# Kernel tuning notes

Hardware: AMD Instinct MI355X
Metric: run time of the kernel (lower is better)

The kernel has to match this reference:

```python
import jax, jax.numpy as jnp
import numpy as np

# Model dims (from CerebroOriginal defaults)
B, C, T, E, H, NB, NC = 256, 14, 8, 180, 5, 6, 4
DH = E // H          # 36
S = C * T            # 112 tokens
MLP = 4 * E          # 720


def qdq(x):
    """Int8 per-tensor fake quant-dequant (Brevitas Int8ActPerTensorFloat-style), STE."""
    s = jnp.maximum(jnp.max(jnp.abs(x)) / 127.0, 1e-8)
    y = jnp.clip(jnp.round(x / s), -128.0, 127.0) * s
    return x + jax.lax.stop_gradient(y - x)


def ln(x, g, b):
    m = jnp.mean(x, axis=-1, keepdims=True)
    v = jnp.var(x, axis=-1, keepdims=True)
    return (x - m) * jax.lax.rsqrt(v + 1e-5) * g + b


def qlinear(x, w, b):
    """QuantLinear: int8 input quant + int8 per-tensor weight quant, float bias."""
    return qdq(x) @ qdq(w).T + b


def setup_inputs() -> dict:
    key = jax.random.key(0)
    ks = jax.random.split(key, 16)
    r = lambda k, sh: (0.05 * jax.random.normal(k, sh)).astype(jnp.float32)
    f32 = jnp.float32
    return {
        "x": jax.random.normal(ks[0], (B, C, T), dtype=f32),
        "proj_w": r(ks[1], (E, C)), "proj_b": jnp.zeros((E,), f32),
        "ln1_g": jnp.ones((NB, E), f32), "ln1_b": jnp.zeros((NB, E), f32),
        "wq": r(ks[2], (NB, E, E)), "bq": jnp.zeros((NB, E), f32),
        "wk": r(ks[3], (NB, E, E)), "bk": jnp.zeros((NB, E), f32),
        "wv": r(ks[4], (NB, E, E)), "bv": jnp.zeros((NB, E), f32),
        "wo": r(ks[5], (NB, E, E)), "bo": jnp.zeros((NB, E), f32),
        "ln2_g": jnp.ones((NB, E), f32), "ln2_b": jnp.zeros((NB, E), f32),
        "fc1_w": r(ks[6], (NB, MLP, E)), "fc1_b": jnp.zeros((NB, MLP), f32),
        "fc2_w": r(ks[7], (NB, E, MLP)), "fc2_b": jnp.zeros((NB, E), f32),
        "fn_g": jnp.ones((E,), f32), "fn_b": jnp.zeros((E,), f32),
        "cls_w": r(ks[8], (NC, E)), "cls_b": jnp.zeros((NC,), f32),
    }


def forward(x, proj_w, proj_b, ln1_g, ln1_b, wq, bq, wk, bk, wv, bv, wo, bo,
            ln2_g, ln2_b, fc1_w, fc1_b, fc2_w, fc2_b, fn_g, fn_b, cls_w, cls_b):
    # input quant -> [B,T,C] -> proj -> [B,T,E]
    h = jnp.transpose(qdq(x), (0, 2, 1))
    h = qlinear(h, proj_w, proj_b)
    # expand over channels then flatten to [B, C*T, E] (channel-major token layout)
    h = jnp.broadcast_to(h[:, None], (B, C, T, E)).reshape(B, S, E)

    for i in range(NB):
        # --- attention sub-block ---
        r1 = h
        a = qdq(ln(h, ln1_g[i], ln1_b[i])).reshape(B, C, T, E)
        if i % 2 == 0:  # temporal attention: attend over T within each channel
            a = a.reshape(B * C, T, E)
            L = T
        else:           # channel attention: attend over C within each time step
            a = jnp.transpose(a, (0, 2, 1, 3)).reshape(B * T, C, E)
            L = C
        q = qlinear(a, wq[i], bq[i]).reshape(-1, L, H, DH)
        k = qlinear(a, wk[i], bk[i]).reshape(-1, L, H, DH)
        v = qlinear(a, wv[i], bv[i]).reshape(-1, L, H, DH)
        scores = jnp.einsum('nlhd,nmhd->nhlm', q, k) / jnp.sqrt(jnp.float32(DH))
        att = jax.nn.softmax(scores, axis=-1)
        o = jnp.einsum('nhlm,nmhd->nlhd', att, v).reshape(-1, L, E)
        o = qlinear(o, wo[i], bo[i])
        if i % 2 == 0:
            o = o.reshape(B, C, T, E)
        else:
            o = jnp.transpose(o.reshape(B, T, C, E), (0, 2, 1, 3))
        h = r1 + o.reshape(B, S, E)

        # --- MLP sub-block ---
        r2 = h
        m = qdq(ln(h, ln2_g[i], ln2_b[i]))
        m = qlinear(m, fc1_w[i], fc1_b[i])
        m = qdq(jax.nn.gelu(m))
        m = qlinear(m, fc2_w[i], fc2_b[i])
        h = r2 + m

    h = qdq(ln(h, fn_g, fn_b))
    pooled = jnp.mean(h, axis=1)                 # QuantMean over tokens -> [B, E]
    return qlinear(pooled, cls_w, cls_b)         # [B, NC]


def reference(x, proj_w, proj_b, ln1_g, ln1_b, wq, bq, wk, bk, wv, bv, wo, bo,
              ln2_g, ln2_b, fc1_w, fc1_b, fc2_w, fc2_b, fn_g, fn_b, cls_w, cls_b):
    return forward(x, proj_w, proj_b, ln1_g, ln1_b, wq, bq, wk, bk, wv, bv, wo, bo,
                   ln2_g, ln2_b, fc1_w, fc1_b, fc2_w, fc2_b, fn_g, fn_b, cls_w, cls_b)
```

## Files before the change

### kernel.cpp

```cpp
#include <hip/hip_runtime.h>
#include <math.h>

#define E 180
#define S 112
#define Bb 256
#define CC 14
#define TT 8
#define HH 5
#define DH 36
#define NBLK 6
#define MLPD 720
#define M_TOK (Bb*S)
#define BUF ((size_t)M_TOK * E)

#define KP1 192
#define KP2 736

#define WQ8_OFF   0
#define WK8_OFF   36864
#define WV8_OFF   73728
#define WO8_OFF   110592
#define FC18_OFF  147456
#define FC28_OFF  285696
#define WBLK      427008

#define SLOT_X    0
#define SLOT_PW   1
#define SLOT_CW   2
#define SLOT_POOL 3
#define SLOT_FLN  4
#define SLOT_WQ   8
#define SLOT_WK   16
#define SLOT_WV   24
#define SLOT_WO   32
#define SLOT_FC1  40
#define SLOT_FC2  48
#define SLOT_LN1  56
#define SLOT_O    64
#define SLOT_LN2  72
#define SLOT_GELU 80
#define SLOT_GXMAX 88
#define SLOT_GXA   96
#define SLOT_GXB   104
#define SLOT_GDIR  112

#define XL (-0.7535)
#define XR (-0.7515)

typedef unsigned long long ull;
typedef __attribute__((ext_vector_type(8))) short short8;
typedef __attribute__((ext_vector_type(4))) float f32x4;

__device__ __forceinline__ double slot_scale(const ull* s){
  return fmax(__longlong_as_double((long long)*s) / 127.0, 1e-8);
}
__device__ __forceinline__ void atomic_max_d(ull* p, double v){
  atomicMax(p, (ull)__double_as_longlong(v));
}
__device__ __forceinline__ ull enc_d(double d){
  ull b = (ull)__double_as_longlong(d);
  return (b >> 63) ? ~b : (b | 0x8000000000000000ULL);
}
__device__ __forceinline__ double dec_d(ull k){
  ull b = (k >> 63) ? (k ^ 0x8000000000000000ULL) : ~k;
  return __longlong_as_double((long long)b);
}
__device__ __forceinline__ float q_int_d(double x, double s){
  double r = rint(x / s);
  r = fmin(fmax(r, -128.0), 127.0);
  return (float)r;
}
__device__ __forceinline__ float q_int_fast(double x, double s, float sf){
  float t = (float)x / sf;
  float r = rintf(t);
  if(fabsf(t - r) > 0.497f || fabsf(t) > 126.f){
    double rd = rint(x / s);
    rd = fmin(fmax(rd, -128.0), 127.0);
    return (float)rd;
  }
  return r;
}
__device__ __forceinline__ unsigned short f2bf(float f){
  return (unsigned short)(__float_as_uint(f) >> 16);
}
__device__ __forceinline__ double gelu_d(double x){
  double t = tanh(0.7978845608028654*(x + 0.044715*x*x*x));
  return 0.5*x*(1.0 + t);
}
__device__ __forceinline__ float gelu_f(float x){
  float t = tanhf(0.7978845608f*(x + 0.044715f*x*x*x));
  return 0.5f*x*(1.f + t);
}
__device__ __forceinline__ int pmap(int row, int mode){
  if(mode == 0) return row;
  int b = row / S; int r = row - b*S; int t = r / CC; int c = r - t*CC;
  return b*S + c*TT + t;
}
__device__ __forceinline__ int pmap_inv(int row){
  int b = row / S; int r = row - b*S; int c = r / TT; int t = r - c*TT;
  return b*S + t*CC + c;
}

__global__ void init_slots(ull* slots){
  int t = threadIdx.x;
  slots[t] = (t >= SLOT_GXB && t < SLOT_GXB + NBLK) ? ~0ULL : 0ULL;
}

__global__ void amax_f32(const float* __restrict__ src, int seglen, ull* slots){
  int seg = blockIdx.y;
  const float* p = src + (size_t)seg * seglen;
  float m = 0.f;
  for(int i = blockIdx.x*256 + threadIdx.x; i < seglen; i += gridDim.x*256)
    m = fmaxf(m, fabsf(p[i]));
  __shared__ float red[256];
  red[threadIdx.x] = m;
  __syncthreads();
  for(int off = 128; off > 0; off >>= 1){
    if(threadIdx.x < off) red[threadIdx.x] = fmaxf(red[threadIdx.x], red[threadIdx.x+off]);
    __syncthreads();
  }
  if(threadIdx.x == 0) atomic_max_d(slots + seg, (double)red[0]);
}

__global__ void quant_w(const float* __restrict__ src, int N, int K,
                        int Npad, int Kpad, const ull* __restrict__ slotbase,
                        unsigned short* __restrict__ dst, size_t dstoff){
  int i = blockIdx.y;
  int e = blockIdx.x*256 + threadIdx.x;
  int tot = Npad * Kpad;
  if(e >= tot) return;
  int n = e / Kpad, k = e - n*Kpad;
  double s = slot_scale(slotbase + i);
  float val = 0.f;
  if(n < N && k < K)
    val = q_int_d((double)src[(size_t)i*N*K + (size_t)n*K + k], s);
  dst[(size_t)i*WBLK + dstoff + e] = f2bf(val);
}

__global__ void proj_bcast(const float* __restrict__ x, const float* __restrict__ pw,
                           const float* __restrict__ pb, double* __restrict__ h,
                           const ull* __restrict__ sx_slot,
                           const ull* __restrict__ sw_slot){
  int tid = blockIdx.x*256 + threadIdx.x;
  if(tid >= Bb*TT*E) return;
  int e = tid % E; int bt = tid / E; int t = bt % TT; int b = bt / TT;
  double sx = slot_scale(sx_slot), sw = slot_scale(sw_slot);
  float acc = 0.f;
  for(int c = 0; c < CC; c++)
    acc += q_int_d((double)x[(b*CC + c)*TT + t], sx) * q_int_d((double)pw[e*CC + c], sw);
  double o = (double)acc * (sx * sw) + (double)pb[e];
  for(int c = 0; c < CC; c++)
    h[((size_t)b*S + c*TT + t)*E + e] = o;
}

__device__ __forceinline__ void ln_row(const double* __restrict__ in, size_t base, int lane,
    const float* __restrict__ g, const float* __restrict__ bta,
    double& y0, double& y1, double& y2){
  double x0 = in[base + lane];
  double x1 = in[base + lane + 64];
  double x2 = (lane < E - 128) ? in[base + lane + 128] : 0.0;
  double sum = x0 + x1 + x2;
  for(int m = 32; m > 0; m >>= 1) sum += __shfl_xor(sum, m);
  double mean = sum * (1.0 / E);
  double d0 = x0 - mean, d1 = x1 - mean;
  double d2 = (lane < E - 128) ? (x2 - mean) : 0.0;
  double vs = d0*d0 + d1*d1 + d2*d2;
  for(int m = 32; m > 0; m >>= 1) vs += __shfl_xor(vs, m);
  double inv = 1.0 / sqrt(vs * (1.0 / E) + 1e-5);
  y0 = d0*inv*(double)g[lane]      + (double)bta[lane];
  y1 = d1*inv*(double)g[lane+64]   + (double)bta[lane+64];
  y2 = (lane < E - 128) ? (d2*inv*(double)g[lane+128] + (double)bta[lane+128]) : 0.0;
}

template<bool WRITE>
__global__ void __launch_bounds__(256) ln_amax(const double* __restrict__ in,
    double* __restrict__ out, const float* __restrict__ g,
    const float* __restrict__ bta, ull* amax_slot){
  int wave = threadIdx.x >> 6, lane = threadIdx.x & 63;
  double amx = 0.0;
  for(int tok = blockIdx.x*4 + wave; tok < M_TOK; tok += gridDim.x*4){
    size_t base = (size_t)tok * E;
    double y0, y1, y2;
    ln_row(in, base, lane, g, bta, y0, y1, y2);
    if(WRITE){
      out[base + lane]      = y0;
      out[base + lane + 64] = y1;
      if(lane < E - 128) out[base + lane + 128] = y2;
    }
    amx = fmax(amx, fmax(fabs(y0), fabs(y1)));
    if(lane < E - 128) amx = fmax(amx, fabs(y2));
  }
  for(int m = 32; m > 0; m >>= 1) amx = fmax(amx, __shfl_xor(amx, m));
  __shared__ double red[4];
  if(lane == 0) red[wave] = amx;
  __syncthreads();
  if(threadIdx.x == 0){
    double m = fmax(fmax(red[0], red[1]), fmax(red[2], red[3]));
    atomic_max_d(amax_slot, m);
  }
}

template<int PERM>
__global__ void __launch_bounds__(256) ln_quant(const double* __restrict__ in,
    unsigned short* __restrict__ dst, const float* __restrict__ g,
    const float* __restrict__ bta, const ull* __restrict__ slot){
  int wave = threadIdx.x >> 6, lane = threadIdx.x & 63;
  double s = slot_scale(slot); float sf = (float)s;
  for(int tok = blockIdx.x*4 + wave; tok < M_TOK; tok += gridDim.x*4){
    size_t base = (size_t)tok * E;
    double y0, y1, y2;
    ln_row(in, base, lane, g, bta, y0, y1, y2);
    int d = PERM ? pmap_inv(tok) : tok;
    unsigned short* dr = dst + (size_t)d*KP1;
    dr[lane]       = f2bf(q_int_fast(y0, s, sf));
    dr[lane + 64]  = f2bf(q_int_fast(y1, s, sf));
    dr[lane + 128] = (lane < E - 128) ? f2bf(q_int_fast(y2, s, sf)) : (unsigned short)0;
  }
}

__global__ void __launch_bounds__(256) quant_act(const double* __restrict__ src,
                          unsigned short* __restrict__ dst,
                          const ull* __restrict__ slot){
  int tid = blockIdx.x*256 + threadIdx.x;
  if(tid >= M_TOK*KP1/8) return;
  int idx8 = tid*8;
  int row = idx8 / KP1, k0 = idx8 - row*KP1;
  double s = slot_scale(slot); float sf = (float)s;
  const double* sp = src + (size_t)row*E;
  unsigned short v[8];
  #pragma unroll
  for(int j = 0; j < 8; j++){
    int k = k0 + j;
    v[j] = (k < E) ? f2bf(q_int_fast(sp[k], s, sf)) : (unsigned short)0;
  }
  *reinterpret_cast<short8*>(dst + (size_t)row*KP1 + k0) = *reinterpret_cast<short8*>(v);
}

__global__ void __launch_bounds__(256) quant_mid(const float* __restrict__ midacc,
                          unsigned short* __restrict__ dst,
                          const ull* __restrict__ slotA, const ull* __restrict__ slotW,
                          const ull* __restrict__ slotG, const float* __restrict__ bias){
  int tid = blockIdx.x*256 + threadIdx.x;
  if(tid >= M_TOK*KP2/8) return;
  int idx8 = tid*8;
  int row = idx8 / KP2, k0 = idx8 - row*KP2;
  double sAW = slot_scale(slotA) * slot_scale(slotW);
  double sg = slot_scale(slotG);
  float sAWf = (float)sAW, sgf = (float)sg;
  const float* sp = midacc + (size_t)row*MLPD;
  unsigned short v[8];
  #pragma unroll
  for(int j = 0; j < 8; j++){
    int k = k0 + j;
    if(k < MLPD){
      float a = sp[k];
      float y = fmaf(a, sAWf, bias[k]);
      float gf = gelu_f(y);
      float t = gf / sgf;
      float r = rintf(t);
      if(fabsf(t - r) > 0.497f || fabsf(t) > 126.f){
        double outv = (double)a*sAW + (double)bias[k];
        double rd = rint(gelu_d(outv)/sg);
        rd = fmin(fmax(rd, -128.0), 127.0);
        r = (float)rd;
      }
      v[j] = f2bf(r);
    } else v[j] = 0;
  }
  *reinterpret_cast<short8*>(dst + (size_t)row*KP2 + k0) = *reinterpret_cast<short8*>(v);
}

__global__ void gelu_finalize(ull* slots, int i){
  if(threadIdx.x != 0) return;
  double am = 0.0;
  ull kx = slots[SLOT_GXMAX + i];
  if(kx){ double x = dec_d(kx); if(fabs(x) < 1e299) am = fabs(gelu_d(x)); }
  ull ka = slots[SLOT_GXA + i];
  if(ka){ double x = dec_d(ka); if(fabs(x) < 1e299) am = fmax(am, fabs(gelu_d(x))); }
  ull kb = slots[SLOT_GXB + i];
  if(kb != ~0ULL){ double x = dec_d(kb); if(fabs(x) < 1e299) am = fmax(am, fabs(gelu_d(x))); }
  am = fmax(am, __longlong_as_double((long long)slots[SLOT_GDIR + i]));
  slots[SLOT_GELU + i] = (ull)__double_as_longlong(am);
}

__global__ void __launch_bounds__(256) gemm_qkv(
    const unsigned short* __restrict__ A8,
    const unsigned short* __restrict__ Wq, float* __restrict__ outq)
{
  int sel = blockIdx.x;
  const unsigned short* W8 = Wq + (size_t)sel*36864;
  float* outF = outq + (size_t)sel*((size_t)M_TOK*E);
  int wave = threadIdx.x >> 6, lane = threadIdx.x & 63;
  int m0 = blockIdx.y*64 + wave*16;
  int lr = lane & 15, lg = lane >> 4;
  const unsigned short* Arow = A8 + (size_t)(m0 + lr)*KP1 + lg*8;
  const unsigned short* Wbase = W8 + (size_t)lr*KP1 + lg*8;
  f32x4 acc[12];
  #pragma unroll
  for(int j = 0; j < 12; j++) acc[j] = (f32x4){0.f,0.f,0.f,0.f};
  for(int kk = 0; kk < KP1/32; kk++){
    short8 a = *reinterpret_cast<const short8*>(Arow + kk*32);
    const unsigned short* Wp = Wbase + kk*32;
    #pragma unroll
    for(int j = 0; j < 12; j++){
      short8 b = *reinterpret_cast<const short8*>(Wp + (size_t)j*16*KP1);
      acc[j] = __builtin_amdgcn_mfma_f32_16x16x32_bf16(a, b, acc[j], 0, 0, 0);
    }
  }
  #pragma unroll
  for(int j = 0; j < 12; j++){
    int col = j*16 + lr;
    if(col >= E) continue;
    #pragma unroll
    for(int r = 0; r < 4; r++){
      int row = m0 + lg*4 + r;
      outF[(size_t)row*E + col] = acc[j][r];
    }
  }
}

template<int NT, int EPI>
__global__ void __launch_bounds__(256) gemm_mfma(
    const unsigned short* __restrict__ A8, int Kpad,
    const unsigned short* __restrict__ W8,
    const float* __restrict__ bias, int Nreal,
    float* __restrict__ outF, double* __restrict__ outH,
    const ull* __restrict__ slotA, const ull* __restrict__ slotW,
    ull* cand, int permOut)
{
  int wave = threadIdx.x >> 6, lane = threadIdx.x & 63;
  int m0 = blockIdx.y*64 + wave*16;
  int tbase = blockIdx.x*NT;
  int lr = lane & 15, lg = lane >> 4;
  const unsigned short* Arow = A8 + (size_t)(m0 + lr)*Kpad + lg*8;
  const unsigned short* Wbase = W8 + (size_t)(tbase*16 + lr)*Kpad + lg*8;
  f32x4 acc[NT];
  #pragma unroll
  for(int j = 0; j < NT; j++) acc[j] = (f32x4){0.f,0.f,0.f,0.f};
  int ksteps = Kpad >> 5;
  for(int kk = 0; kk < ksteps; kk++){
    short8 a = *reinterpret_cast<const short8*>(Arow + kk*32);
    const unsigned short* Wp = Wbase + kk*32;
    #pragma unroll
    for(int j = 0; j < NT; j++){
      short8 b = *reinterpret_cast<const short8*>(Wp + (size_t)j*16*Kpad);
      acc[j] = __builtin_amdgcn_mfma_f32_16x16x32_bf16(a, b, acc[j], 0, 0, 0);
    }
  }
  double sAW = slot_scale(slotA) * slot_scale(slotW);
  double xmax = -1e300, xa = -1e300, xb = 1e300, dir = 0.0;
  #pragma unroll
  for(int j = 0; j < NT; j++){
    int col = (tbase + j)*16 + lr;
    if(col >= Nreal) continue;
    #pragma unroll
    for(int r = 0; r < 4; r++){
      int row = m0 + lg*4 + r;
      float a = acc[j][r];
      if(EPI == 0){
        outF[(size_t)row*Nreal + col] = a;
      } else if(EPI == 1){
        double outv = (double)a * sAW + (double)bias[col];
        int orow = pmap(row, permOut);
        size_t idx = (size_t)orow*E + col;
        outH[idx] += outv;
      } else {
        double outv = (double)a * sAW + (double)bias[col];
        outF[(size_t)row*Nreal + col] = a;
        xmax = fmax(xmax, outv);
        if(outv <= XL) xa = fmax(xa, outv);
        else if(outv < XR) dir = fmax(dir, fabs(gelu_d(outv)));
        if(outv >= XR) xb = fmin(xb, outv);
      }
    }
  }
  if(EPI == 2){
    for(int m = 32; m > 0; m >>= 1){
      xmax = fmax(xmax, __shfl_xor(xmax, m));
      xa   = fmax(xa,   __shfl_xor(xa,   m));
      xb   = fmin(xb,   __shfl_xor(xb,   m));
      dir  = fmax(dir,  __shfl_xor(dir,  m));
    }
    __shared__ double r0[4], r1[4], r2[4], r3[4];
    if(lane == 0){ r0[wave]=xmax; r1[wave]=xa; r2[wave]=xb; r3[wave]=dir; }
    __syncthreads();
    if(threadIdx.x == 0){
      double M0=r0[0], A0=r1[0], B0=r2[0], D0=r3[0];
      for(int w = 1; w < 4; w++){
        M0 = fmax(M0, r0[w]); A0 = fmax(A0, r1[w]);
        B0 = fmin(B0, r2[w]); D0 = fmax(D0, r3[w]);
      }
      atomicMax(cand + SLOT_GXMAX, enc_d(M0));
      atomicMax(cand + SLOT_GXA,   enc_d(A0));
      atomicMin(cand + SLOT_GXB,   enc_d(B0));
      atomicMax(cand + SLOT_GDIR,  (ull)__double_as_longlong(D0));
    }
  }
}

__global__ void __launch_bounds__(64) attn_kernel(const float* __restrict__ qa,
    const float* __restrict__ ka, const float* __restrict__ va,
    double* __restrict__ o, int L,
    const float* __restrict__ bq, const float* __restrict__ bk,
    const float* __restrict__ bv,
    const ull* __restrict__ sLN, const ull* __restrict__ sWq,
    const ull* __restrict__ sWk, const ull* __restrict__ sWv,
    ull* amax_slot){
  __shared__ double qs[14*36], ks[14*36], vs[14*36];
  __shared__ double att[14*14];
  int tid = threadIdx.x;
  double sA = slot_scale(sLN);
  double dq = sA * slot_scale(sWq);
  double dk = sA * slot_scale(sWk);
  double dv = sA * slot_scale(sWv);
  double am = 0.0;
  for(int gseg = 0; gseg < 8; gseg++){
    int segid = blockIdx.x*8 + gseg;
    int n = segid / HH, hh = segid % HH;
    size_t rowbase = (size_t)n*L*E + hh*DH;
    for(int idx = tid; idx < L*DH; idx += 64){
      int l = idx / DH, d = idx - l*DH;
      size_t g = rowbase + (size_t)l*E + d;
      int bcol = hh*DH + d;
      qs[idx] = (double)qa[g]*dq + (double)bq[bcol];
      ks[idx] = (double)ka[g]*dk + (double)bk[bcol];
      vs[idx] = (double)va[g]*dv + (double)bv[bcol];
    }
    __syncthreads();
    for(int idx = tid; idx < L*L; idx += 64){
      int l = idx / L, m = idx - l*L;
      double s = 0.0;
      for(int d = 0; d < DH; d++) s += qs[l*DH+d] * ks[m*DH+d];
      att[idx] = s * (1.0 / 6.0);
    }
    __syncthreads();
    if(tid < L){
      double mx = -1e300;
      for(int m = 0; m < L; m++) mx = fmax(mx, att[tid*L+m]);
      double sm = 0.0;
      for(int m = 0; m < L; m++){ double e_ = exp(att[tid*L+m] - mx); att[tid*L+m] = e_; sm += e_; }
      double r = 1.0 / sm;
      for(int m = 0; m < L; m++) att[tid*L+m] *= r;
    }
    __syncthreads();
    for(int idx = tid; idx < L*DH; idx += 64){
      int l = idx / DH, d = idx - l*DH;
      double s = 0.0;
      for(int m = 0; m < L; m++) s += att[l*L+m] * vs[m*DH+d];
      o[rowbase + (size_t)l*E + d] = s;
      am = fmax(am, fabs(s));
    }
    __syncthreads();
  }
  for(int m = 32; m > 0; m >>= 1) am = fmax(am, __shfl_xor(am, m));
  if(tid == 0) atomic_max_d(amax_slot, am);
}

__global__ void __launch_bounds__(256) pooled_kernel(const double* __restrict__ lnout,
    double* __restrict__ pooled, const ull* __restrict__ slot_ln,
    ull* slot_pooled){
  int tid = blockIdx.x*256 + threadIdx.x;
  double am = 0.0;
  if(tid < Bb*E){
    int b = tid / E, e = tid - (tid/E)*E;
    double sl = slot_scale(slot_ln); float slf = (float)sl;
    double sum = 0.0;
    for(int s = 0; s < S; s++)
      sum += (double)q_int_fast(lnout[((size_t)b*S + s)*E + e], sl, slf) * sl;
    double pv = sum * (1.0 / S);
    pooled[(size_t)b*E + e] = pv;
    am = fabs(pv);
  }
  for(int m = 32; m > 0; m >>= 1) am = fmax(am, __shfl_xor(am, m));
  if((threadIdx.x & 63) == 0) atomic_max_d(slot_pooled, am);
}

__global__ void __launch_bounds__(64) cls_kernel(const double* __restrict__ pooled,
    const float* __restrict__ cw, const float* __restrict__ cb,
    float* __restrict__ out, const ull* __restrict__ sp,
    const ull* __restrict__ sw){
  int tid = blockIdx.x*64 + threadIdx.x;
  if(tid >= Bb*4) return;
  int b = tid >> 2, j = tid & 3;
  double s1 = slot_scale(sp), s2 = slot_scale(sw);
  float acc = 0.f;
  for(int e = 0; e < E; e++)
    acc += q_int_d(pooled[b*E + e], s1) * q_int_d((double)cw[j*E + e], s2);
  out[tid] = (float)((double)acc * (s1 * s2) + (double)cb[j]);
}

extern "C" void kernel_launch(void* const* d_in, const int* in_sizes, int n_in,
                              void* d_out, int out_size, void* d_ws, size_t ws_size,
                              hipStream_t stream){
  const float* x      = (const float*)d_in[0];
  const float* proj_w = (const float*)d_in[1];
  const float* proj_b = (const float*)d_in[2];
  const float* ln1_g  = (const float*)d_in[3];
  const float* ln1_b  = (const float*)d_in[4];
  const float* wq     = (const float*)d_in[5];
  const float* bq     = (const float*)d_in[6];
  const float* wk     = (const float*)d_in[7];
  const float* bk     = (const float*)d_in[8];
  const float* wv     = (const float*)d_in[9];
  const float* bv     = (const float*)d_in[10];
  const float* wo     = (const float*)d_in[11];
  const float* bo     = (const float*)d_in[12];
  const float* ln2_g  = (const float*)d_in[13];
  const float* ln2_b  = (const float*)d_in[14];
  const float* fc1_w  = (const float*)d_in[15];
  const float* fc1_b  = (const float*)d_in[16];
  const float* fc2_w  = (const float*)d_in[17];
  const float* fc2_b  = (const float*)d_in[18];
  const float* fn_g   = (const float*)d_in[19];
  const float* fn_b   = (const float*)d_in[20];
  const float* cls_w  = (const float*)d_in[21];
  const float* cls_b  = (const float*)d_in[22];
  float* outp = (float*)d_out;

  char* base = (char*)d_ws;
  ull*    slots  = (ull*)base;
  double* h      = (double*)(base + 4096);
  double* scr    = h + BUF;
  float*  facc   = (float*)(scr + BUF);
  float*  qacc   = facc;
  float*  midacc = facc;
  double* pooled = (double*)facc;
  unsigned short* act8 = (unsigned short*)(facc + (size_t)M_TOK*MLPD);
  unsigned short* mid8 = act8 + (size_t)M_TOK*KP1;
  unsigned short* w8   = mid8 + (size_t)M_TOK*KP2;

  init_slots<<<1, 128, 0, stream>>>(slots);

  amax_f32<<<dim3(32,1), 256, 0, stream>>>(x,      Bb*CC*TT, slots + SLOT_X);
  amax_f32<<<dim3(1,1),  256, 0, stream>>>(proj_w, E*CC,     slots + SLOT_PW);
  amax_f32<<<dim3(1,1),  256, 0, stream>>>(cls_w,  4*E,      slots + SLOT_CW);
  amax_f32<<<dim3(4,NBLK),  256, 0, stream>>>(wq,    E*E,    slots + SLOT_WQ);
  amax_f32<<<dim3(4,NBLK),  256, 0, stream>>>(wk,    E*E,    slots + SLOT_WK);
  amax_f32<<<dim3(4,NBLK),  256, 0, stream>>>(wv,    E*E,    slots + SLOT_WV);
  amax_f32<<<dim3(4,NBLK),  256, 0, stream>>>(wo,    E*E,    slots + SLOT_WO);
  amax_f32<<<dim3(16,NBLK), 256, 0, stream>>>(fc1_w, MLPD*E, slots + SLOT_FC1);
  amax_f32<<<dim3(16,NBLK), 256, 0, stream>>>(fc2_w, MLPD*E, slots + SLOT_FC2);

  quant_w<<<dim3((KP1*KP1+255)/256, NBLK), 256, 0, stream>>>(wq, E, E, KP1, KP1, slots+SLOT_WQ, w8, WQ8_OFF);
  quant_w<<<dim3((KP1*KP1+255)/256, NBLK), 256, 0, stream>>>(wk, E, E, KP1, KP1, slots+SLOT_WK, w8, WK8_OFF);
  quant_w<<<dim3((KP1*KP1+255)/256, NBLK), 256, 0, stream>>>(wv, E, E, KP1, KP1, slots+SLOT_WV, w8, WV8_OFF);
  quant_w<<<dim3((KP1*KP1+255)/256, NBLK), 256, 0, stream>>>(wo, E, E, KP1, KP1, slots+SLOT_WO, w8, WO8_OFF);
  quant_w<<<dim3((MLPD*KP1+255)/256, NBLK), 256, 0, stream>>>(fc1_w, MLPD, E, MLPD, KP1, slots+SLOT_FC1, w8, FC18_OFF);
  quant_w<<<dim3((KP1*KP2+255)/256, NBLK), 256, 0, stream>>>(fc2_w, E, MLPD, KP1, KP2, slots+SLOT_FC2, w8, FC28_OFF);

  proj_bcast<<<(Bb*TT*E + 255)/256, 256, 0, stream>>>(x, proj_w, proj_b, h,
                                                      slots + SLOT_X, slots + SLOT_PW);

  const int QA_GRID = (M_TOK*KP1/8 + 255)/256;
  const int QM_GRID = (M_TOK*KP2/8 + 255)/256;
  const int LN_GRID = 1792;

  for(int i = 0; i < NBLK; i++){
    int pi = i & 1;
    const unsigned short* wb = w8 + (size_t)i*WBLK;
    ln_amax<false><<<LN_GRID, 256, 0, stream>>>(h, nullptr, ln1_g + i*E, ln1_b + i*E, slots + SLOT_LN1 + i);
    if(pi == 0)
      ln_quant<0><<<LN_GRID, 256, 0, stream>>>(h, act8, ln1_g + i*E, ln1_b + i*E, slots + SLOT_LN1 + i);
    else
      ln_quant<1><<<LN_GRID, 256, 0, stream>>>(h, act8, ln1_g + i*E, ln1_b + i*E, slots + SLOT_LN1 + i);
    gemm_qkv<<<dim3(3, M_TOK/64), 256, 0, stream>>>(act8, wb + WQ8_OFF, qacc);
    int L = pi ? CC : TT;
    int nseg = (M_TOK/L)*HH;
    attn_kernel<<<nseg/8, 64, 0, stream>>>(qacc, qacc + (size_t)M_TOK*E, qacc + (size_t)2*M_TOK*E, scr, L,
        bq + i*E, bk + i*E, bv + i*E,
        slots+SLOT_LN1+i, slots+SLOT_WQ+i, slots+SLOT_WK+i, slots+SLOT_WV+i,
        slots + SLOT_O + i);
    quant_act<<<QA_GRID, 256, 0, stream>>>(scr, act8, slots + SLOT_O + i);
    gemm_mfma<12,1><<<dim3(1, M_TOK/64), 256, 0, stream>>>(act8, KP1, wb + WO8_OFF, bo + i*E, E,
        nullptr, h, slots+SLOT_O+i, slots+SLOT_WO+i, nullptr, pi);
    ln_amax<false><<<LN_GRID, 256, 0, stream>>>(h, nullptr, ln2_g + i*E, ln2_b + i*E, slots + SLOT_LN2 + i);
    ln_quant<0><<<LN_GRID, 256, 0, stream>>>(h, act8, ln2_g + i*E, ln2_b + i*E, slots + SLOT_LN2 + i);
    gemm_mfma<9,2><<<dim3(5, M_TOK/64), 256, 0, stream>>>(act8, KP1, wb + FC18_OFF, fc1_b + i*MLPD, MLPD,
        midacc, nullptr, slots+SLOT_LN2+i, slots+SLOT_FC1+i, slots + i, 0);
    gelu_finalize<<<1, 64, 0, stream>>>(slots, i);
    quant_mid<<<QM_GRID, 256, 0, stream>>>(midacc, mid8,
        slots+SLOT_LN2+i, slots+SLOT_FC1+i, slots+SLOT_GELU+i, fc1_b + i*MLPD);
    gemm_mfma<12,1><<<dim3(1, M_TOK/64), 256, 0, stream>>>(mid8, KP2, wb + FC28_OFF, fc2_b + i*E, E,
        nullptr, h, slots+SLOT_GELU+i, slots+SLOT_FC2+i, nullptr, 0);
  }

  ln_amax<true><<<LN_GRID, 256, 0, stream>>>(h, scr, fn_g, fn_b, slots + SLOT_FLN);
  pooled_kernel<<<(Bb*E + 255)/256, 256, 0, stream>>>(scr, pooled, slots + SLOT_FLN, slots + SLOT_POOL);
  cls_kernel<<<(Bb*4 + 63)/64, 64, 0, stream>>>(pooled, cls_w, cls_b, outp,
                                                slots + SLOT_POOL, slots + SLOT_CW);
}
```

Before: 3.880 ms.

## Fuse LayerNorm amax into residual GEMM epilogue and rewrite attention kernel

The residual-add GEMM epilogue (Wo and fc2) now computes the updated row, its LayerNorm, and the max-abs for the next LayerNorm's quant scale, then publishes it atomically. This removes the separate ln_amax passes over h inside the loop. Attention is templated on sequence length, stores Q/K/V in float shared memory, folds the dequant scale and bias algebraically into the score computation, pads the score rows, and handles 4 segments per block instead of 8. The risks are extra register pressure in the GEMM epilogue, because each row is kept in doubles for the reductions, and small numerical differences from the rearranged bias algebra.

Result: faster. 3.634 ms (-6.3%).

```diff
diff --git a/kernel.cpp b/kernel.cpp
--- a/kernel.cpp
+++ b/kernel.cpp
@@ -326,7 +326,8 @@
     const float* __restrict__ bias, int Nreal,
     float* __restrict__ outF, double* __restrict__ outH,
     const ull* __restrict__ slotA, const ull* __restrict__ slotW,
-    ull* cand, int permOut)
+    ull* cand, int permOut,
+    const float* __restrict__ lng, const float* __restrict__ lnb)
 {
   int wave = threadIdx.x >> 6, lane = threadIdx.x & 63;
   int m0 = blockIdx.y*64 + wave*16;
@@ -348,23 +349,25 @@
     }
   }
   double sAW = slot_scale(slotA) * slot_scale(slotW);
-  double xmax = -1e300, xa = -1e300, xb = 1e300, dir = 0.0;
-  #pragma unroll
-  for(int j = 0; j < NT; j++){
-    int col = (tbase + j)*16 + lr;
-    if(col >= Nreal) continue;
+  if(EPI == 0){
     #pragma unroll
-    for(int r = 0; r < 4; r++){
-      int row = m0 + lg*4 + r;
-      float a = acc[j][r];
-      if(EPI == 0){
-        outF[(size_t)row*Nreal + col] = a;
-      } else if(EPI == 1){
-        double outv = (double)a * sAW + (double)bias[col];
-        int orow = pmap(row, permOut);
-        size_t idx = (size_t)orow*E + col;
-        outH[idx] += outv;
-      } else {
+    for(int j = 0; j < NT; j++){
+      int col = (tbase + j)*16 + lr;
+      if(col >= Nreal) continue;
+      #pragma unroll
+      for(int r = 0; r < 4; r++)
+        outF[(size_t)(m0 + lg*4 + r)*Nreal + col] = acc[j][r];
+    }
+  } else if(EPI == 2){
+    double xmax = -1e300, xa = -1e300, xb = 1e300, dir = 0.0;
+    #pragma unroll
+    for(int j = 0; j < NT; j++){
+      int col = (tbase + j)*16 + lr;
+      if(col >= Nreal) continue;
+      #pragma unroll
+      for(int r = 0; r < 4; r++){
+        int row = m0 + lg*4 + r;
+        float a = acc[j][r];
         double outv = (double)a * sAW + (double)bias[col];
         outF[(size_t)row*Nreal + col] = a;
         xmax = fmax(xmax, outv);
@@ -373,8 +376,6 @@
         if(outv >= XR) xb = fmin(xb, outv);
       }
     }
-  }
-  if(EPI == 2){
     for(int m = 32; m > 0; m >>= 1){
       xmax = fmax(xmax, __shfl_xor(xmax, m));
       xa   = fmax(xa,   __shfl_xor(xa,   m));
@@ -395,58 +396,128 @@
       atomicMin(cand + SLOT_GXB,   enc_d(B0));
       atomicMax(cand + SLOT_GDIR,  (ull)__double_as_longlong(D0));
     }
-  }
-}
-
-__global__ void __launch_bounds__(64) attn_kernel(const float* __restrict__ qa,
+  } else {
+    double amx = 0.0;
+    #pragma unroll
+    for(int r = 0; r < 4; r++){
+      int row = m0 + lg*4 + r;
+      int orow = pmap(row, permOut);
+      double hvr[NT];
+      double rsum = 0.0;
+      #pragma unroll
+      for(int j = 0; j < NT; j++){
+        int col = j*16 + lr;
+        double nh = 0.0;
+        if(col < Nreal){
+          double outv = (double)acc[j][r] * sAW + (double)bias[col];
+          size_t idx = (size_t)orow*E + col;
+          nh = outH[idx] + outv;
+          outH[idx] = nh;
+        }
+        hvr[j] = nh;
+        rsum += nh;
+      }
+      for(int m = 1; m <= 8; m <<= 1) rsum += __shfl_xor(rsum, m);
+      double mean = rsum * (1.0 / E);
+      double vsum = 0.0;
+      #pragma unroll
+      for(int j = 0; j < NT; j++){
+        int col = j*16 + lr;
+        double d_ = (col < Nreal) ? (hvr[j] - mean) : 0.0;
+        vsum += d_*d_;
+      }
+      for(int m = 1; m <= 8; m <<= 1) vsum += __shfl_xor(vsum, m);
+      double inv = 1.0 / sqrt(vsum * (1.0 / E) + 1e-5);
+      #pragma unroll
+      for(int j = 0; j < NT; j++){
+        int col = j*16 + lr;
+        if(col < Nreal){
+          double y = (hvr[j] - mean)*inv*(double)lng[col] + (double)lnb[col];
+          amx = fmax(amx, fabs(y));
+        }
+      }
+    }
+    for(int m = 1; m <= 32; m <<= 1) amx = fmax(amx, __shfl_xor(amx, m));
+    __shared__ double redA[4];
+    if(lane == 0) redA[wave] = amx;
+    __syncthreads();
+    if(threadIdx.x == 0)
+      atomic_max_d(cand, fmax(fmax(redA[0], redA[1]), fmax(redA[2], redA[3])));
+  }
+}
+
+template<int L>
+__global__ void __launch_bounds__(64) attn_v2(const float* __restrict__ qa,
     const float* __restrict__ ka, const float* __restrict__ va,
-    double* __restrict__ o, int L,
+    double* __restrict__ o,
     const float* __restrict__ bq, const float* __restrict__ bk,
     const float* __restrict__ bv,
     const ull* __restrict__ sLN, const ull* __restrict__ sWq,
     const ull* __restrict__ sWk, const ull* __restrict__ sWv,
     ull* amax_slot){
-  __shared__ double qs[14*36], ks[14*36], vs[14*36];
-  __shared__ double att[14*14];
+  const int LP = L + 1;
+  __shared__ float qs[L*DH], kT[DH*L], vs[L*DH];
+  __shared__ double att[L*LP];
+  __shared__ double QB[L], KB[L], BBs;
   int tid = threadIdx.x;
   double sA = slot_scale(sLN);
   double dq = sA * slot_scale(sWq);
   double dk = sA * slot_scale(sWk);
   double dv = sA * slot_scale(sWv);
+  double dqk = dq * dk;
   double am = 0.0;
-  for(int gseg = 0; gseg < 8; gseg++){
-    int segid = blockIdx.x*8 + gseg;
+  for(int gseg = 0; gseg < 4; gseg++){
+    int segid = blockIdx.x*4 + gseg;
     int n = segid / HH, hh = segid % HH;
     size_t rowbase = (size_t)n*L*E + hh*DH;
+    const float* bqh = bq + hh*DH;
+    const float* bkh = bk + hh*DH;
+    const float* bvh = bv + hh*DH;
     for(int idx = tid; idx < L*DH; idx += 64){
       int l = idx / DH, d = idx - l*DH;
       size_t g = rowbase + (size_t)l*E + d;
-      int bcol = hh*DH + d;
-      qs[idx] = (double)qa[g]*dq + (double)bq[bcol];
-      ks[idx] = (double)ka[g]*dk + (double)bk[bcol];
-      vs[idx] = (double)va[g]*dv + (double)bv[bcol];
+      float qv = qa[g], kv = ka[g], vv = va[g];
+      qs[l*DH+d] = qv;
+      kT[d*L+l]  = kv;
+      vs[l*DH+d] = vv;
+    }
+    __syncthreads();
+    if(tid < L){
+      double s = 0.0;
+      for(int d = 0; d < DH; d++) s += (double)qs[tid*DH+d] * (double)bkh[d];
+      QB[tid] = s;
+    } else if(tid >= 16 && tid < 16 + L){
+      int m = tid - 16;
+      double s = 0.0;
+      for(int d = 0; d < DH; d++) s += (double)kT[d*L+m] * (double)bqh[d];
+      KB[m] = s;
+    } else if(tid == 63){
+      double s = 0.0;
+      for(int d = 0; d < DH; d++) s += (double)bqh[d] * (double)bkh[d];
+      BBs = s;
     }
     __syncthreads();
     for(int idx = tid; idx < L*L; idx += 64){
       int l = idx / L, m = idx - l*L;
-      double s = 0.0;
-      for(int d = 0; d < DH; d++) s += qs[l*DH+d] * ks[m*DH+d];
-      att[idx] = s * (1.0 / 6.0);
+      double si = 0.0;
+      for(int d = 0; d < DH; d++) si += (double)qs[l*DH+d] * (double)kT[d*L+m];
+      att[l*LP+m] = (dqk*si + dq*QB[l] + dk*KB[m] + BBs) * (1.0 / 6.0);
     }
     __syncthreads();
     if(tid < L){
       double mx = -1e300;
-      for(int m = 0; m < L; m++) mx = fmax(mx, att[tid*L+m]);
+      for(int m = 0; m < L; m++) mx = fmax(mx, att[tid*LP+m]);
       double sm = 0.0;
-      for(int m = 0; m < L; m++){ double e_ = exp(att[tid*L+m] - mx); att[tid*L+m] = e_; sm += e_; }
+      for(int m = 0; m < L; m++){ double e_ = exp(att[tid*LP+m] - mx); att[tid*LP+m] = e_; sm += e_; }
       double r = 1.0 / sm;
-      for(int m = 0; m < L; m++) att[tid*L+m] *= r;
+      for(int m = 0; m < L; m++) att[tid*LP+m] *= r;
     }
     __syncthreads();
     for(int idx = tid; idx < L*DH; idx += 64){
       int l = idx / DH, d = idx - l*DH;
+      double bvd = (double)bvh[d];
       double s = 0.0;
-      for(int m = 0; m < L; m++) s += att[l*L+m] * vs[m*DH+d];
+      for(int m = 0; m < L; m++) s += att[l*LP+m] * ((double)vs[m*DH+d]*dv + bvd);
       o[rowbase + (size_t)l*E + d] = s;
       am = fmax(am, fabs(s));
     }
@@ -555,33 +626,44 @@
   const int QM_GRID = (M_TOK*KP2/8 + 255)/256;
   const int LN_GRID = 1792;
 
+  ln_amax<false><<<LN_GRID, 256, 0, stream>>>(h, nullptr, ln1_g, ln1_b, slots + SLOT_LN1);
+
   for(int i = 0; i < NBLK; i++){
     int pi = i & 1;
     const unsigned short* wb = w8 + (size_t)i*WBLK;
-    ln_amax<false><<<LN_GRID, 256, 0, stream>>>(h, nullptr, ln1_g + i*E, ln1_b + i*E, slots + SLOT_LN1 + i);
     if(pi == 0)
       ln_quant<0><<<LN_GRID, 256, 0, stream>>>(h, act8, ln1_g + i*E, ln1_b + i*E, slots + SLOT_LN1 + i);
     else
       ln_quant<1><<<LN_GRID, 256, 0, stream>>>(h, act8, ln1_g + i*E, ln1_b + i*E, slots + SLOT_LN1 + i);
     gemm_qkv<<<dim3(3, M_TOK/64), 256, 0, stream>>>(act8, wb + WQ8_OFF, qacc);
-    int L = pi ? CC : TT;
-    int nseg = (M_TOK/L)*HH;
-    attn_kernel<<<nseg/8, 64, 0, stream>>>(qacc, qacc + (size_t)M_TOK*E, qacc + (size_t)2*M_TOK*E, scr, L,
-        bq + i*E, bk + i*E, bv + i*E,
-        slots+SLOT_LN1+i, slots+SLOT_WQ+i, slots+SLOT_WK+i, slots+SLOT_WV+i,
-        slots + SLOT_O + i);
+    if(pi == 0){
+      int nseg = (M_TOK/TT)*HH;
+      attn_v2<TT><<<nseg/4, 64, 0, stream>>>(qacc, qacc + (size_t)M_TOK*E, qacc + (size_t)2*M_TOK*E, scr,
+          bq + i*E, bk + i*E, bv + i*E,
+          slots+SLOT_LN1+i, slots+SLOT_WQ+i, slots+SLOT_WK+i, slots+SLOT_WV+i,
+          slots + SLOT_O + i);
+    } else {
+      int nseg = (M_TOK/CC)*HH;
+      attn_v2<CC><<<nseg/4, 64, 0, stream>>>(qacc, qacc + (size_t)M_TOK*E, qacc + (size_t)2*M_TOK*E, scr,
+          bq + i*E, bk + i*E, bv + i*E,
+          slots+SLOT_LN1+i, slots+SLOT_WQ+i, slots+SLOT_WK+i, slots+SLOT_WV+i,
+          slots + SLOT_O + i);
+    }
     quant_act<<<QA_GRID, 256, 0, stream>>>(scr, act8, slots + SLOT_O + i);
-    gemm_mfma<12,1><<<dim3(1, M_TOK/64), 256, 0, stream>>>(act8, KP1, wb + WO8_OFF, bo + i*E, E,
-        nullptr, h, slots+SLOT_O+i, slots+SLOT_WO+i, nullptr, pi);
-    ln_amax<false><<<LN_GRID, 256, 0, stream>>>(h, nullptr, ln2_g + i*E, ln2_b + i*E, slots + SLOT_LN2 + i);
+    gemm_mfma<12,3><<<dim3(1, M_TOK/64), 256, 0, stream>>>(act8, KP1, wb + WO8_OFF, bo + i*E, E,
+        nullptr, h, slots+SLOT_O+i, slots+SLOT_WO+i, slots+SLOT_LN2+i, pi,
+        ln2_g + i*E, ln2_b + i*E);
     ln_quant<0><<<LN_GRID, 256, 0, stream>>>(h, act8, ln2_g + i*E, ln2_b + i*E, slots + SLOT_LN2 + i);
     gemm_mfma<9,2><<<dim3(5, M_TOK/64), 256, 0, stream>>>(act8, KP1, wb + FC18_OFF, fc1_b + i*MLPD, MLPD,
-        midacc, nullptr, slots+SLOT_LN2+i, slots+SLOT_FC1+i, slots + i, 0);
+        midacc, nullptr, slots+SLOT_LN2+i, slots+SLOT_FC1+i, slots + i, 0, nullptr, nullptr);
     gelu_finalize<<<1, 64, 0, stream>>>(slots, i);
     quant_mid<<<QM_GRID, 256, 0, stream>>>(midacc, mid8,
         slots+SLOT_LN2+i, slots+SLOT_FC1+i, slots+SLOT_GELU+i, fc1_b + i*MLPD);
-    gemm_mfma<12,1><<<dim3(1, M_TOK/64), 256, 0, stream>>>(mid8, KP2, wb + FC28_OFF, fc2_b + i*E, E,
-        nullptr, h, slots+SLOT_GELU+i, slots+SLOT_FC2+i, nullptr, 0);
+    ull* nslot = (i < 5) ? (slots + SLOT_LN1 + i + 1) : (slots + SLOT_FLN);
+    const float* ng = (i < 5) ? (ln1_g + (i+1)*E) : fn_g;
+    const float* nb = (i < 5) ? (ln1_b + (i+1)*E) : fn_b;
+    gemm_mfma<12,3><<<dim3(1, M_TOK/64), 256, 0, stream>>>(mid8, KP2, wb + FC28_OFF, fc2_b + i*E, E,
+        nullptr, h, slots+SLOT_GELU+i, slots+SLOT_FC2+i, nslot, 0, ng, nb);
   }
 
   ln_amax<true><<<LN_GRID, 256, 0, stream>>>(h, scr, fn_g, fn_b, slots + SLOT_FLN);
```
